# Kernel optimization log

Hardware: AMD Instinct MI355X
Metric: run time of the kernel (lower is better)

Reference implementation:

```python
import jax, jax.numpy as jnp
import numpy as np

L = 12        # depth
DIM = 768     # model dim
HEADS = 12
DHEAD = 64
INNER = HEADS * DHEAD   # 768
MLP = 3072
P = 16        # patch size
IMG = 384
C = 3
B = 16
NCLS = 1000
NPATCH = (IMG // P) ** 2   # 576
N = NPATCH + 1             # 577 (cls token)
PATCH_DIM = C * P * P      # 768
SCALE = DIM ** (-0.5)      # NOTE: original scales by dim, not dim_head


def setup_inputs() -> dict:
    key = jax.random.key(0)
    ks = jax.random.split(key, 21)
    rn = lambda k, shape, s=0.02: jax.random.normal(k, shape, dtype=jnp.float32) * s
    return {
        "img": jax.random.normal(ks[0], (B, C, IMG, IMG), dtype=jnp.float32),
        "patch_w": rn(ks[1], (PATCH_DIM, DIM)),
        "patch_b": rn(ks[2], (DIM,)),
        "pos_emb": rn(ks[3], (1, N, DIM), 1.0),
        "cls_tok": rn(ks[4], (1, 1, DIM), 1.0),
        "ln1_w": jnp.ones((L, DIM), jnp.float32),
        "ln1_b": jnp.zeros((L, DIM), jnp.float32),
        "qkv_w": rn(ks[5], (L, DIM, 3 * INNER)),
        "out_w": rn(ks[6], (L, INNER, DIM)),
        "out_b": rn(ks[7], (L, DIM)),
        "ln2_w": jnp.ones((L, DIM), jnp.float32),
        "ln2_b": jnp.zeros((L, DIM), jnp.float32),
        "ff1_w": rn(ks[8], (L, DIM, MLP)),
        "ff1_b": rn(ks[9], (L, MLP)),
        "ff2_w": rn(ks[10], (L, MLP, DIM)),
        "ff2_b": rn(ks[11], (L, DIM)),
        "head_ln_w": jnp.ones((DIM,), jnp.float32),
        "head_ln_b": jnp.zeros((DIM,), jnp.float32),
        "head_w": rn(ks[12], (DIM, NCLS)),
        "head_b": rn(ks[13], (NCLS,)),
    }


def layer_norm(x, w, b, eps=1e-5):
    mu = jnp.mean(x, axis=-1, keepdims=True)
    var = jnp.mean(jnp.square(x - mu), axis=-1, keepdims=True)
    return (x - mu) * jax.lax.rsqrt(var + eps) * w + b


def _vit_forward(img, patch_w, patch_b, pos_emb, cls_tok,
                 ln1_w, ln1_b, qkv_w, out_w, out_b,
                 ln2_w, ln2_b, ff1_w, ff1_b, ff2_w, ff2_b,
                 head_ln_w, head_ln_b, head_w, head_b):
    b = img.shape[0]
    g = IMG // P
    # rearrange 'b c (h p1) (w p2) -> b (h w) (p1 p2 c)'
    x = img.reshape(b, C, g, P, g, P).transpose(0, 2, 4, 3, 5, 1).reshape(b, NPATCH, PATCH_DIM)
    x = x @ patch_w + patch_b                           # [b, 576, dim]
    cls = jnp.broadcast_to(cls_tok, (b, 1, DIM))
    x = jnp.concatenate([cls, x], axis=1) + pos_emb[:, :N]   # [b, 577, dim]

    def block(x, p):
        l1w, l1b, qkvw, ow, ob, l2w, l2b, f1w, f1b, f2w, f2b = p
        # attention (pre-norm, residual inside Attention.forward)
        h = layer_norm(x, l1w, l1b)
        qkv = h @ qkvw                                  # [b, n, 3*inner]
        q, k, v = jnp.split(qkv, 3, axis=-1)
        to_heads = lambda t: t.reshape(b, N, HEADS, DHEAD).transpose(0, 2, 1, 3)
        q, k, v = to_heads(q), to_heads(k), to_heads(v)  # [b, h, n, d]
        dots = jnp.einsum('bhid,bhjd->bhij', q, k) * SCALE
        attn = jax.nn.softmax(dots, axis=-1)
        o = jnp.einsum('bhij,bhjd->bhid', attn, v)
        o = o.transpose(0, 2, 1, 3).reshape(b, N, INNER)
        x = x + (o @ ow + ob)
        # feedforward (pre-norm, residual)
        h2 = layer_norm(x, l2w, l2b)
        h2 = jax.nn.gelu(h2 @ f1w + f1b, approximate=False)
        x = x + (h2 @ f2w + f2b)
        return x, None

    x, _ = jax.lax.scan(block, x,
                        (ln1_w, ln1_b, qkv_w, out_w, out_b,
                         ln2_w, ln2_b, ff1_w, ff1_b, ff2_w, ff2_b))
    cls_out = x[:, 0]                                   # [b, dim]
    return layer_norm(cls_out, head_ln_w, head_ln_b) @ head_w + head_b


def reference(img, patch_w, patch_b, pos_emb, cls_tok,
              ln1_w, ln1_b, qkv_w, out_w, out_b,
              ln2_w, ln2_b, ff1_w, ff1_b, ff2_w, ff2_b,
              head_ln_w, head_ln_b, head_w, head_b):
    return _vit_forward(img, patch_w, patch_b, pos_emb, cls_tok,
                        ln1_w, ln1_b, qkv_w, out_w, out_b,
                        ln2_w, ln2_b, ff1_w, ff1_b, ff2_w, ff2_b,
                        head_ln_w, head_ln_b, head_w, head_b)
```

## Files before the change

### kernel.cpp

```cpp
#include <hip/hip_runtime.h>
#include <cstdint>


typedef __attribute__((ext_vector_type(8))) short bf16x8;
typedef __attribute__((ext_vector_type(4))) float f32x4;

#define NTOK 577

__device__ __forceinline__ ushort f2bf(float f) {
  union { float f; unsigned int u; } x; x.f = f;
  unsigned int r = x.u + 0x7fffu + ((x.u >> 16) & 1u);
  return (ushort)(r >> 16);
}

__device__ __forceinline__ void gload_lds16(const ushort* g, ushort* l) {
  __builtin_amdgcn_global_load_lds(
      (const __attribute__((address_space(1))) unsigned int*)g,
      (__attribute__((address_space(3))) unsigned int*)l, 16, 0, 0);
}

#define VMCNT4 asm volatile("s_waitcnt vmcnt(4)" ::: "memory")
#define VMCNT2 asm volatile("s_waitcnt vmcnt(2)" ::: "memory")
#define VMCNT0 asm volatile("s_waitcnt vmcnt(0)" ::: "memory")
#define LGKM0  asm volatile("s_waitcnt lgkmcnt(0)" ::: "memory")
#define SCHED0 __builtin_amdgcn_sched_barrier(0)
#define BARRIER __builtin_amdgcn_s_barrier()

__device__ __forceinline__ int gsw(int row) {
  return (row & 7) + 2 * ((row >> 4) & 3);
}

__device__ __forceinline__ void transpose_tile(const float* __restrict__ W,
                                               ushort* __restrict__ Wt,
                                               int K, int N, int kb, int nb,
                                               int tx, int ty, float t[32][33]) {
#pragma unroll
  for (int i = 0; i < 32; i += 8)
    t[ty + i][tx] = W[(size_t)(kb + ty + i) * N + (nb + tx)];
  __syncthreads();
#pragma unroll
  for (int i = 0; i < 32; i += 8)
    Wt[(size_t)(nb + ty + i) * K + (kb + tx)] = f2bf(t[tx][ty + i]);
}

__global__ __launch_bounds__(256) void convt_kernel(const float* __restrict__ W,
                                                    ushort* __restrict__ Wt,
                                                    int K, int N) {
  __shared__ float t[32][33];
  transpose_tile(W, Wt, K, N, blockIdx.x * 32, blockIdx.y * 32,
                 threadIdx.x & 31, threadIdx.x >> 5, t);
}

__global__ __launch_bounds__(256) void wconv_kernel(
    const float* __restrict__ qkv_w, const float* __restrict__ out_w,
    const float* __restrict__ ff1_w, const float* __restrict__ ff2_w,
    ushort* __restrict__ wq, ushort* __restrict__ wo,
    ushort* __restrict__ w1, ushort* __restrict__ w2) {
  __shared__ float t[32][33];
  const int tx = threadIdx.x & 31, ty = threadIdx.x >> 5;
  int bx = blockIdx.x;
  if (bx < 1728) {
    transpose_tile(qkv_w, wq, 768, 2304, (bx % 24) * 32, (bx / 24) * 32, tx, ty, t);
  } else if (bx < 2304) {
    bx -= 1728;
    transpose_tile(out_w, wo, 768, 768, (bx % 24) * 32, (bx / 24) * 32, tx, ty, t);
  } else if (bx < 4608) {
    bx -= 2304;
    transpose_tile(ff1_w, w1, 768, 3072, (bx % 24) * 32, (bx / 24) * 32, tx, ty, t);
  } else {
    bx -= 4608;
    transpose_tile(ff2_w, w2, 3072, 768, (bx % 96) * 32, (bx / 96) * 32, tx, ty, t);
  }
}

__global__ __launch_bounds__(256) void im2col_kernel(const float* __restrict__ img,
                                                     ushort* __restrict__ Ap) {
  const int idx = blockIdx.x * 256 + threadIdx.x;
  const int j = idx % 768;
  const int m = idx / 768;
  const int c = j % 3;
  const int q = j / 3;
  const int px = q & 15, py = q >> 4;
  const int b = m / 576, p = m % 576;
  const int gy = p / 24, gx = p % 24;
  const float v = img[((size_t)(b * 3 + c) * 384 + (gy * 16 + py)) * 384 + (gx * 16 + px)];
  Ap[idx] = f2bf(v);
}

__global__ void clspos_kernel(const float* __restrict__ cls_tok,
                              const float* __restrict__ pos,
                              float* __restrict__ x) {
  const int i = blockIdx.x * 256 + threadIdx.x;
  const int b = i / 768, d = i % 768;
  x[(size_t)b * NTOK * 768 + d] = cls_tok[d] + pos[d];
}

__global__ __launch_bounds__(256) void ln_kernel(const float* __restrict__ x,
                                                 const float* __restrict__ w,
                                                 const float* __restrict__ bb,
                                                 ushort* __restrict__ out) {
  const int wave = threadIdx.x >> 6, lane = threadIdx.x & 63;
  const int row = blockIdx.x * 4 + wave;
  const float4* xr = reinterpret_cast<const float4*>(x + (size_t)row * 768);
  const float4 v0 = xr[lane], v1 = xr[lane + 64], v2 = xr[lane + 128];
  float vals[12] = {v0.x, v0.y, v0.z, v0.w, v1.x, v1.y, v1.z, v1.w,
                    v2.x, v2.y, v2.z, v2.w};
  float s = 0.f;
#pragma unroll
  for (int i = 0; i < 12; ++i) s += vals[i];
#pragma unroll
  for (int o = 32; o; o >>= 1) s += __shfl_xor(s, o);
  const float mu = s * (1.0f / 768.0f);
  float q = 0.f;
#pragma unroll
  for (int i = 0; i < 12; ++i) { const float d = vals[i] - mu; q += d * d; }
#pragma unroll
  for (int o = 32; o; o >>= 1) q += __shfl_xor(q, o);
  const float rstd = rsqrtf(q * (1.0f / 768.0f) + 1e-5f);
  const float4* w4 = reinterpret_cast<const float4*>(w);
  const float4* b4 = reinterpret_cast<const float4*>(bb);
  ushort* orow = out + (size_t)row * 768;
#pragma unroll
  for (int ch = 0; ch < 3; ++ch) {
    const float4 wv = w4[lane + ch * 64];
    const float4 bv = b4[lane + ch * 64];
    ushort4 u;
    u.x = f2bf((vals[ch * 4 + 0] - mu) * rstd * wv.x + bv.x);
    u.y = f2bf((vals[ch * 4 + 1] - mu) * rstd * wv.y + bv.y);
    u.z = f2bf((vals[ch * 4 + 2] - mu) * rstd * wv.z + bv.z);
    u.w = f2bf((vals[ch * 4 + 3] - mu) * rstd * wv.w + bv.w);
    *reinterpret_cast<ushort4*>(orow + ch * 256 + lane * 4) = u;
  }
}

constexpr int EPI_BF16 = 0;
constexpr int EPI_GELU_BF16 = 1;
constexpr int EPI_RES_F32 = 2;
constexpr int EPI_PATCH = 3;

template <int EPI>
__global__ __launch_bounds__(512, 2) void gemm8_kernel(
    const ushort* __restrict__ A, const ushort* __restrict__ Bt,
    const float* __restrict__ bias, void* __restrict__ Cptr,
    int M, int N, int K, int nt) {
  __shared__ ushort lds[2][2][16384];

  const int nwg = gridDim.x;
  const int orig = blockIdx.x;
  const int q8 = nwg >> 3, r8 = nwg & 7, xcd = orig & 7, sidx = orig >> 3;
  const int wg = (xcd < r8 ? xcd * (q8 + 1) : r8 * (q8 + 1) + (xcd - r8) * q8) + sidx;
  const int tileM = (wg / nt) * 256;
  const int tileN = (wg % nt) * 256;

  const int tid = threadIdx.x;
  const int wave = tid >> 6, lane = tid & 63;
  const int wm = wave >> 2, wn = wave & 3;
  const int lr = lane & 15, lg = lane >> 4;

  f32x4 acc[8][4];
#pragma unroll
  for (int i = 0; i < 8; ++i)
#pragma unroll
    for (int j = 0; j < 4; ++j) acc[i][j] = (f32x4){0.f, 0.f, 0.f, 0.f};

  int rsA[2][2], rsB[2][2];
  const ushort* pA[2][2];
  const ushort* pB[2][2];
#pragma unroll
  for (int h = 0; h < 2; ++h)
#pragma unroll
    for (int g = 0; g < 2; ++g) {
      const int c = wave * 2 + g;
      {
        const int rowst = h * 64 + ((c >> 3) << 7) + ((c & 7) << 3);
        rsA[h][g] = rowst;
        const int row = rowst + (lane >> 3);
        const int lgr = ((lane & 7) - gsw(row)) & 7;
        pA[h][g] = A + (size_t)(tileM + row) * K + lgr * 8;
      }
      {
        const int rowst = h * 32 + ((c >> 2) << 6) + ((c & 3) << 3);
        rsB[h][g] = rowst;
        const int row = rowst + (lane >> 3);
        const int lgr = ((lane & 7) - gsw(row)) & 7;
        pB[h][g] = Bt + (size_t)(tileN + row) * K + lgr * 8;
      }
    }

#define STAGE_A(h, buf, k1)                                   \
  gload_lds16(pA[h][0] + (k1), &lds[buf][0][rsA[h][0] * 64]); \
  gload_lds16(pA[h][1] + (k1), &lds[buf][0][rsA[h][1] * 64]);
#define STAGE_B(h, buf, k1)                                   \
  gload_lds16(pB[h][0] + (k1), &lds[buf][1][rsB[h][0] * 64]); \
  gload_lds16(pB[h][1] + (k1), &lds[buf][1][rsB[h][1] * 64]);

  bf16x8 areg[8], breg[4];
#define LDA8(h, buf)                                                          \
  {                                                                           \
    const ushort* base = &lds[buf][0][0];                                     \
    _Pragma("unroll") for (int mf = 0; mf < 4; ++mf) {                        \
      const int row = wm * 128 + (h) * 64 + mf * 16 + lr;                     \
      _Pragma("unroll") for (int ks = 0; ks < 2; ++ks) {                      \
        const int pg = (ks * 4 + lg + (lr & 7) + 2 * mf) & 7;                 \
        areg[mf * 2 + ks] =                                                   \
            *reinterpret_cast<const bf16x8*>(&base[row * 64 + pg * 8]);       \
      }                                                                       \
    }                                                                         \
  }
#define LDB4(q, buf)                                                          \
  {                                                                           \
    const ushort* base = &lds[buf][1][0];                                     \
    _Pragma("unroll") for (int nf = 0; nf < 2; ++nf) {                        \
      const int row = wn * 64 + (q) * 32 + nf * 16 + lr;                      \
      _Pragma("unroll") for (int ks = 0; ks < 2; ++ks) {                      \
        const int pg = (ks * 4 + lg + (lr & 7) + 2 * (((q)*2 + nf) & 3)) & 7; \
        breg[nf * 2 + ks] =                                                   \
            *reinterpret_cast<const bf16x8*>(&base[row * 64 + pg * 8]);       \
      }                                                                       \
    }                                                                         \
  }
#define MFMA16(h, q)                                                        \
  __builtin_amdgcn_s_setprio(1);                                            \
  _Pragma("unroll") for (int mf = 0; mf < 4; ++mf)                          \
      _Pragma("unroll") for (int nf = 0; nf < 2; ++nf)                      \
          _Pragma("unroll") for (int ks = 0; ks < 2; ++ks)                  \
              acc[(h)*4 + mf][(q)*2 + nf] =                                 \
                  __builtin_amdgcn_mfma_f32_16x16x32_bf16(                  \
                      areg[mf * 2 + ks], breg[nf * 2 + ks],                 \
                      acc[(h)*4 + mf][(q)*2 + nf], 0, 0, 0);                \
  __builtin_amdgcn_s_setprio(0);

  STAGE_A(0, 0, 0);
  STAGE_B(0, 0, 0);
  STAGE_A(1, 0, 0);
  STAGE_B(1, 0, 0);

  const int NT = K >> 6;
  for (int t = 0; t < NT - 1; ++t) {
    const int cb = t & 1, nb = (t + 1) & 1;
    const int k1 = (t + 1) * 64;
    VMCNT4; SCHED0;
    BARRIER;
    LDA8(0, cb);
    LDB4(0, cb);
    STAGE_A(0, nb, k1);
    LGKM0; SCHED0;
    MFMA16(0, 0);
    VMCNT4; SCHED0;
    BARRIER;
    LDA8(1, cb);
    STAGE_B(0, nb, k1);
    LGKM0; SCHED0;
    MFMA16(1, 0);
    VMCNT4; SCHED0;
    BARRIER;
    LDB4(1, cb);
    STAGE_A(1, nb, k1);
    LGKM0; SCHED0;
    MFMA16(1, 1);
    BARRIER;
    LDA8(0, cb);
    STAGE_B(1, nb, k1);
    LGKM0; SCHED0;
    MFMA16(0, 1);
  }

  {
    const int cb = (NT - 1) & 1;
    VMCNT4; SCHED0;
    BARRIER;
    LDA8(0, cb);
    LDB4(0, cb);
    LGKM0; SCHED0;
    MFMA16(0, 0);
    VMCNT2; SCHED0;
    BARRIER;
    LDA8(1, cb);
    LGKM0; SCHED0;
    MFMA16(1, 0);
    VMCNT0; SCHED0;
    BARRIER;
    LDB4(1, cb);
    LGKM0; SCHED0;
    MFMA16(1, 1);
    BARRIER;
    LDA8(0, cb);
    LGKM0; SCHED0;
    MFMA16(0, 1);
  }

#pragma unroll
  for (int am = 0; am < 8; ++am) {
#pragma unroll
    for (int r = 0; r < 4; ++r) {
      const int row = tileM + wm * 128 + (am >> 2) * 64 + (am & 3) * 16 + lg * 4 + r;
      if (row >= M) continue;
#pragma unroll
      for (int an = 0; an < 4; ++an) {
        const int col = tileN + wn * 64 + (an >> 1) * 32 + (an & 1) * 16 + lr;
        float v = acc[am][an][r];
        if constexpr (EPI == EPI_BF16) {
          reinterpret_cast<ushort*>(Cptr)[(size_t)row * N + col] = f2bf(v);
        } else {
          v += bias[col];
          v = 0.5f * v * (1.0f + erff(v * 0.70710678118654752440f));
          reinterpret_cast<ushort*>(Cptr)[(size_t)row * N + col] = f2bf(v);
        }
      }
    }
  }
#undef STAGE_A
#undef STAGE_B
#undef LDA8
#undef LDB4
#undef MFMA16
}

template <int EPI>
__global__ __launch_bounds__(256) void gemmP_kernel(
    const ushort* __restrict__ A, const ushort* __restrict__ Bt,
    const float* __restrict__ bias, const float* __restrict__ extra,
    void* __restrict__ Cptr, int M, int N, int K, int mt) {
  __shared__ ushort ldsA[2][128 * 64];
  __shared__ ushort ldsB[2][128 * 64];

  const int nwg = gridDim.x;
  const int orig = blockIdx.x;
  const int q8 = nwg >> 3, r8 = nwg & 7, xcd = orig & 7, sidx = orig >> 3;
  const int wg = (xcd < r8 ? xcd * (q8 + 1) : r8 * (q8 + 1) + (xcd - r8) * q8) + sidx;
  const int tileM = (wg % mt) * 128;
  const int tileN = (wg / mt) * 128;

  const int tid = threadIdx.x;
  const int wave = tid >> 6, lane = tid & 63;
  const int wm = wave >> 1, wn = wave & 1;
  const int lr = lane & 15, lg = lane >> 4;

  f32x4 acc[4][4];
#pragma unroll
  for (int m = 0; m < 4; ++m)
#pragma unroll
    for (int n = 0; n < 4; ++n) acc[m][n] = (f32x4){0.f, 0.f, 0.f, 0.f};

  const ushort* pA[4];
  const ushort* pB[4];
  int dst[4];
#pragma unroll
  for (int i = 0; i < 4; ++i) {
    const int c = wave * 4 + i;
    const int rowst = c * 8;
    dst[i] = rowst * 64;
    const int row = rowst + (lane >> 3);
    const int lgr = ((lane & 7) - gsw(row)) & 7;
    pA[i] = A + (size_t)(tileM + row) * K + lgr * 8;
    pB[i] = Bt + (size_t)(tileN + row) * K + lgr * 8;
  }

#define PSTAGE(buf, kk)                              \
  _Pragma("unroll") for (int i = 0; i < 4; ++i)      \
      gload_lds16(pA[i] + (kk), &ldsA[buf][dst[i]]); \
  _Pragma("unroll") for (int i = 0; i < 4; ++i)      \
      gload_lds16(pB[i] + (kk), &ldsB[buf][dst[i]]);

  PSTAGE(0, 0);

  const int NT = K >> 6;
  int cb = 0;
  for (int t = 0; t < NT; ++t) {
    VMCNT0; SCHED0;
    BARRIER;
    if (t + 1 < NT) { PSTAGE(cb ^ 1, (t + 1) * 64); }
    bf16x8 a[8], b[8];
#pragma unroll
    for (int mf = 0; mf < 4; ++mf) {
      const int row = wm * 64 + mf * 16 + lr;
#pragma unroll
      for (int ks = 0; ks < 2; ++ks) {
        const int pg = (ks * 4 + lg + (lr & 7) + 2 * mf) & 7;
        a[mf * 2 + ks] = *reinterpret_cast<const bf16x8*>(&ldsA[cb][row * 64 + pg * 8]);
      }
    }
#pragma unroll
    for (int nf = 0; nf < 4; ++nf) {
      const int row = wn * 64 + nf * 16 + lr;
#pragma unroll
      for (int ks = 0; ks < 2; ++ks) {
        const int pg = (ks * 4 + lg + (lr & 7) + 2 * nf) & 7;
        b[nf * 2 + ks] = *reinterpret_cast<const bf16x8*>(&ldsB[cb][row * 64 + pg * 8]);
      }
    }
    LGKM0; SCHED0;
    __builtin_amdgcn_s_setprio(1);
#pragma unroll
    for (int mf = 0; mf < 4; ++mf)
#pragma unroll
      for (int nf = 0; nf < 4; ++nf)
#pragma unroll
        for (int ks = 0; ks < 2; ++ks)
          acc[mf][nf] = __builtin_amdgcn_mfma_f32_16x16x32_bf16(
              a[mf * 2 + ks], b[nf * 2 + ks], acc[mf][nf], 0, 0, 0);
    __builtin_amdgcn_s_setprio(0);
    cb ^= 1;
  }

#pragma unroll
  for (int mf = 0; mf < 4; ++mf) {
#pragma unroll
    for (int r = 0; r < 4; ++r) {
      const int row = tileM + wm * 64 + mf * 16 + lg * 4 + r;
      if (row >= M) continue;
#pragma unroll
      for (int nf = 0; nf < 4; ++nf) {
        const int col = tileN + wn * 64 + nf * 16 + lr;
        float v = acc[mf][nf][r];
        if constexpr (EPI == EPI_BF16) {
          reinterpret_cast<ushort*>(Cptr)[(size_t)row * N + col] = f2bf(v);
        } else if constexpr (EPI == EPI_GELU_BF16) {
          v += bias[col];
          v = 0.5f * v * (1.0f + erff(v * 0.70710678118654752440f));
          reinterpret_cast<ushort*>(Cptr)[(size_t)row * N + col] = f2bf(v);
        } else if constexpr (EPI == EPI_RES_F32) {
          v += bias[col] + extra[(size_t)row * N + col];
          reinterpret_cast<float*>(Cptr)[(size_t)row * N + col] = v;
        } else {
          const int bb = row / 576;
          const int p = row - bb * 576;
          v += bias[col] + extra[(size_t)(p + 1) * 768 + col];
          reinterpret_cast<float*>(Cptr)[(size_t)(row + bb + 1) * 768 + col] = v;
        }
      }
    }
  }
#undef PSTAGE
}

__global__ __launch_bounds__(256) void attn_kernel(const ushort* __restrict__ qkv,
                                                   ushort* __restrict__ o) {
  __shared__ ushort sK[64 * 64];
  __shared__ ushort sVt[64 * 64];
  __shared__ ushort sP[4][16 * 72];
  const int bh = blockIdx.x;
  const int b = bh / 12, hh = bh % 12;
  const int q0 = blockIdx.y * 64;
  const int tid = threadIdx.x;
  const int wave = tid >> 6, lane = tid & 63;
  const int lr = lane & 15;
  const int lg = lane >> 4;
  const ushort* base = qkv + (size_t)b * NTOK * 2304 + hh * 64;
  const float SC = 0.03608439182435161f;

  bf16x8 qf[2];
  {
    const int qrow = q0 + wave * 16 + lr;
    if (qrow < NTOK) {
      const ushort* qp = base + (size_t)qrow * 2304 + lg * 8;
      qf[0] = *reinterpret_cast<const bf16x8*>(qp);
      qf[1] = *reinterpret_cast<const bf16x8*>(qp + 32);
    } else {
      qf[0] = (bf16x8){0, 0, 0, 0, 0, 0, 0, 0};
      qf[1] = qf[0];
    }
  }

  float mst[4], lst[4];
  f32x4 oacc[4];
#pragma unroll
  for (int i = 0; i < 4; ++i) {
    mst[i] = -1e30f; lst[i] = 0.f;
    oacc[i] = (f32x4){0.f, 0.f, 0.f, 0.f};
  }

  const int skey = tid >> 2;
  const int sc4 = tid & 3;
  const int gswk = gsw(skey);

  for (int t0 = 0; t0 < NTOK; t0 += 64) {
    __syncthreads();
    {
      const int gk = t0 + skey;
      int4 k0v, k1v, v0v, v1v;
      if (gk < NTOK) {
        const int4* kp = reinterpret_cast<const int4*>(base + (size_t)gk * 2304 + 768 + sc4 * 16);
        k0v = kp[0]; k1v = kp[1];
        const int4* vp = reinterpret_cast<const int4*>(base + (size_t)gk * 2304 + 1536 + sc4 * 16);
        v0v = vp[0]; v1v = vp[1];
      } else {
        int4 z; z.x = z.y = z.z = z.w = 0;
        k0v = k1v = v0v = v1v = z;
      }
      *reinterpret_cast<int4*>(&sK[skey * 64 + (((2 * sc4 + 0) + gswk) & 7) * 8]) = k0v;
      *reinterpret_cast<int4*>(&sK[skey * 64 + (((2 * sc4 + 1) + gswk) & 7) * 8]) = k1v;
      const ushort* vs = reinterpret_cast<const ushort*>(&v0v);
      const ushort* vs2 = reinterpret_cast<const ushort*>(&v1v);
#pragma unroll
      for (int i = 0; i < 8; ++i) {
        const int d0 = sc4 * 16 + i;
        const int pg0 = ((skey >> 3) + gsw(d0)) & 7;
        sVt[d0 * 64 + pg0 * 8 + (skey & 7)] = vs[i];
        const int d1 = sc4 * 16 + 8 + i;
        const int pg1 = ((skey >> 3) + gsw(d1)) & 7;
        sVt[d1 * 64 + pg1 * 8 + (skey & 7)] = vs2[i];
      }
    }
    __syncthreads();

    f32x4 sacc[4];
#pragma unroll
    for (int n = 0; n < 4; ++n) sacc[n] = (f32x4){0.f, 0.f, 0.f, 0.f};
#pragma unroll
    for (int n = 0; n < 4; ++n) {
      const int row = n * 16 + lr;
      const int rot = (lr & 7) + 2 * n;
      const bf16x8 kf0 = *reinterpret_cast<const bf16x8*>(&sK[row * 64 + ((lg + rot) & 7) * 8]);
      const bf16x8 kf1 = *reinterpret_cast<const bf16x8*>(&sK[row * 64 + ((4 + lg + rot) & 7) * 8]);
      sacc[n] = __builtin_amdgcn_mfma_f32_16x16x32_bf16(qf[0], kf0, sacc[n], 0, 0, 0);
      sacc[n] = __builtin_amdgcn_mfma_f32_16x16x32_bf16(qf[1], kf1, sacc[n], 0, 0, 0);
    }

    float s[4][4], pm[4];
#pragma unroll
    for (int reg = 0; reg < 4; ++reg) pm[reg] = -1e30f;
#pragma unroll
    for (int n = 0; n < 4; ++n)
#pragma unroll
      for (int reg = 0; reg < 4; ++reg) {
        float v = sacc[n][reg] * SC;
        if (t0 + n * 16 + lr >= NTOK) v = -1e30f;
        s[n][reg] = v;
        pm[reg] = fmaxf(pm[reg], v);
      }
#pragma unroll
    for (int off = 1; off < 16; off <<= 1)
#pragma unroll
      for (int reg = 0; reg < 4; ++reg) pm[reg] = fmaxf(pm[reg], __shfl_xor(pm[reg], off));

    float al[4], rs[4];
#pragma unroll
    for (int reg = 0; reg < 4; ++reg) {
      const float mn = fmaxf(mst[reg], pm[reg]);
      al[reg] = __expf(mst[reg] - mn);
      mst[reg] = mn;
      rs[reg] = 0.f;
    }
#pragma unroll
    for (int n = 0; n < 4; ++n)
#pragma unroll
      for (int reg = 0; reg < 4; ++reg) {
        s[n][reg] = __expf(s[n][reg] - mst[reg]);
        rs[reg] += s[n][reg];
      }
#pragma unroll
    for (int off = 1; off < 16; off <<= 1)
#pragma unroll
      for (int reg = 0; reg < 4; ++reg) rs[reg] += __shfl_xor(rs[reg], off);
#pragma unroll
    for (int reg = 0; reg < 4; ++reg) {
      lst[reg] = lst[reg] * al[reg] + rs[reg];
#pragma unroll
      for (int n = 0; n < 4; ++n) oacc[n][reg] *= al[reg];
    }

#pragma unroll
    for (int n = 0; n < 4; ++n)
#pragma unroll
      for (int reg = 0; reg < 4; ++reg)
        sP[wave][(lg * 4 + reg) * 72 + n * 16 + lr] = f2bf(s[n][reg]);

    const bf16x8 pf0 = *reinterpret_cast<const bf16x8*>(&sP[wave][lr * 72 + lg * 8]);
    const bf16x8 pf1 = *reinterpret_cast<const bf16x8*>(&sP[wave][lr * 72 + 32 + lg * 8]);
#pragma unroll
    for (int n = 0; n < 4; ++n) {
      const int row = n * 16 + lr;
      const int rot = (lr & 7) + 2 * n;
      const bf16x8 vf0 = *reinterpret_cast<const bf16x8*>(&sVt[row * 64 + ((lg + rot) & 7) * 8]);
      const bf16x8 vf1 = *reinterpret_cast<const bf16x8*>(&sVt[row * 64 + ((4 + lg + rot) & 7) * 8]);
      oacc[n] = __builtin_amdgcn_mfma_f32_16x16x32_bf16(pf0, vf0, oacc[n], 0, 0, 0);
      oacc[n] = __builtin_amdgcn_mfma_f32_16x16x32_bf16(pf1, vf1, oacc[n], 0, 0, 0);
    }
  }

#pragma unroll
  for (int reg = 0; reg < 4; ++reg) {
    const int q = q0 + wave * 16 + lg * 4 + reg;
    if (q >= NTOK) continue;
    const float inv = 1.0f / lst[reg];
    ushort* op = o + (size_t)(b * NTOK + q) * 768 + hh * 64;
#pragma unroll
    for (int n = 0; n < 4; ++n) op[n * 16 + lr] = f2bf(oacc[n][reg] * inv);
  }
}

__global__ __launch_bounds__(256) void head_kernel(const float* __restrict__ x,
                                                   const float* __restrict__ lw,
                                                   const float* __restrict__ lb,
                                                   const float* __restrict__ hw,
                                                   const float* __restrict__ hb,
                                                   float* __restrict__ out) {
  __shared__ float srow[768];
  __shared__ float sred[8];
  const int b = blockIdx.x, tid = threadIdx.x;
  const float* xr = x + (size_t)b * NTOK * 768;
  for (int i = tid; i < 768; i += 256) srow[i] = xr[i];
  __syncthreads();
  float part = srow[tid] + srow[tid + 256] + srow[tid + 512];
#pragma unroll
  for (int off = 32; off; off >>= 1) part += __shfl_xor(part, off);
  if ((tid & 63) == 0) sred[tid >> 6] = part;
  __syncthreads();
  const float mu = (sred[0] + sred[1] + sred[2] + sred[3]) * (1.0f / 768.0f);
  const float d0 = srow[tid] - mu, d1 = srow[tid + 256] - mu, d2 = srow[tid + 512] - mu;
  float vp = d0 * d0 + d1 * d1 + d2 * d2;
#pragma unroll
  for (int off = 32; off; off >>= 1) vp += __shfl_xor(vp, off);
  if ((tid & 63) == 0) sred[4 + (tid >> 6)] = vp;
  __syncthreads();
  const float rstd = rsqrtf((sred[4] + sred[5] + sred[6] + sred[7]) * (1.0f / 768.0f) + 1e-5f);
  for (int i = tid; i < 768; i += 256) srow[i] = (srow[i] - mu) * rstd * lw[i] + lb[i];
  __syncthreads();
  const int c = blockIdx.y * 250 + tid;
  if (tid < 250 && c < 1000) {
    float a = 0.f;
#pragma unroll 4
    for (int k = 0; k < 768; ++k) a += srow[k] * hw[(size_t)k * 1000 + c];
    out[b * 1000 + c] = a + hb[c];
  }
}

extern "C" void kernel_launch(void* const* d_in, const int* in_sizes, int n_in,
                              void* d_out, int out_size, void* d_ws, size_t ws_size,
                              hipStream_t stream) {
  const float* img     = (const float*)d_in[0];
  const float* patch_w = (const float*)d_in[1];
  const float* patch_b = (const float*)d_in[2];
  const float* pos_emb = (const float*)d_in[3];
  const float* cls_tok = (const float*)d_in[4];
  const float* ln1_w   = (const float*)d_in[5];
  const float* ln1_b   = (const float*)d_in[6];
  const float* qkv_w   = (const float*)d_in[7];
  const float* out_w   = (const float*)d_in[8];
  const float* out_b   = (const float*)d_in[9];
  const float* ln2_w   = (const float*)d_in[10];
  const float* ln2_b   = (const float*)d_in[11];
  const float* ff1_w   = (const float*)d_in[12];
  const float* ff1_b   = (const float*)d_in[13];
  const float* ff2_w   = (const float*)d_in[14];
  const float* ff2_b   = (const float*)d_in[15];
  const float* hln_w   = (const float*)d_in[16];
  const float* hln_b   = (const float*)d_in[17];
  const float* head_w  = (const float*)d_in[18];
  const float* head_b  = (const float*)d_in[19];
  float* outp = (float*)d_out;

  char* wsp = (char*)d_ws;
  auto alloc = [&](size_t bytes) {
    char* p = wsp;
    wsp += (bytes + 255) & ~(size_t)255;
    return p;
  };
  float*  x    = (float*) alloc((size_t)9232 * 768 * 4);
  ushort* h    = (ushort*)alloc((size_t)9232 * 768 * 2);
  ushort* qkvb = (ushort*)alloc((size_t)9232 * 2304 * 2);
  ushort* mlp  = (ushort*)alloc((size_t)9232 * 3072 * 2);
  ushort* wq   = (ushort*)alloc((size_t)768 * 2304 * 2);
  ushort* wo   = (ushort*)alloc((size_t)768 * 768 * 2);
  ushort* w1   = (ushort*)alloc((size_t)768 * 3072 * 2);
  ushort* w2   = (ushort*)alloc((size_t)3072 * 768 * 2);
  ushort* apatch = mlp;
  ushort* wpatch = wq;

  convt_kernel<<<dim3(24, 24), 256, 0, stream>>>(patch_w, wpatch, 768, 768);
  im2col_kernel<<<27648, 256, 0, stream>>>(img, apatch);
  gemmP_kernel<EPI_PATCH><<<72 * 6, 256, 0, stream>>>(
      apatch, wpatch, patch_b, pos_emb, x, 9216, 768, 768, 72);
  clspos_kernel<<<48, 256, 0, stream>>>(cls_tok, pos_emb, x);

  for (int l = 0; l < 12; ++l) {
    wconv_kernel<<<6912, 256, 0, stream>>>(
        qkv_w + (size_t)l * 768 * 2304, out_w + (size_t)l * 768 * 768,
        ff1_w + (size_t)l * 768 * 3072, ff2_w + (size_t)l * 3072 * 768,
        wq, wo, w1, w2);
    ln_kernel<<<2308, 256, 0, stream>>>(x, ln1_w + l * 768, ln1_b + l * 768, h);
    gemm8_kernel<EPI_BF16><<<37 * 9, 512, 0, stream>>>(
        h, wq, nullptr, qkvb, 9232, 2304, 768, 9);
    attn_kernel<<<dim3(192, 10), 256, 0, stream>>>(qkvb, h);
    gemmP_kernel<EPI_RES_F32><<<73 * 6, 256, 0, stream>>>(
        h, wo, out_b + l * 768, x, x, 9232, 768, 768, 73);
    ln_kernel<<<2308, 256, 0, stream>>>(x, ln2_w + l * 768, ln2_b + l * 768, h);
    gemm8_kernel<EPI_GELU_BF16><<<37 * 12, 512, 0, stream>>>(
        h, w1, ff1_b + l * 3072, mlp, 9232, 3072, 768, 12);
    gemmP_kernel<EPI_RES_F32><<<73 * 6, 256, 0, stream>>>(
        mlp, w2, ff2_b + l * 768, x, x, 9232, 768, 3072, 73);
  }

  head_kernel<<<dim3(16, 4), 256, 0, stream>>>(x, hln_w, hln_b, head_w, head_b, outp);
}
```

Measured before the change: 4.171 ms.

## Restructure gemm8 main loop into two phases and split-K the head GEMV

The 8-wave GEMM main loop now loads all B fragments once per k-tile and issues two 32-MFMA phases instead of four 16-MFMA phases. This halves the barriers per tile and changes the global-to-LDS prefetch order and vmcnt waits to match. It adds breg register pressure, which may lower occupancy. Separately, the classifier head kernel splits K across four wave groups with an LDS reduction and launches more blocks, to get more parallelism on the small GEMV.

```diff
diff --git a/kernel.cpp b/kernel.cpp
--- a/kernel.cpp
+++ b/kernel.cpp
@@ -19,7 +19,7 @@
       (__attribute__((address_space(3))) unsigned int*)l, 16, 0, 0);
 }
 
-#define VMCNT4 asm volatile("s_waitcnt vmcnt(4)" ::: "memory")
+#define VMCNT6 asm volatile("s_waitcnt vmcnt(6)" ::: "memory")
 #define VMCNT2 asm volatile("s_waitcnt vmcnt(2)" ::: "memory")
 #define VMCNT0 asm volatile("s_waitcnt vmcnt(0)" ::: "memory")
 #define LGKM0  asm volatile("s_waitcnt lgkmcnt(0)" ::: "memory")
@@ -194,7 +194,7 @@
   gload_lds16(pB[h][0] + (k1), &lds[buf][1][rsB[h][0] * 64]); \
   gload_lds16(pB[h][1] + (k1), &lds[buf][1][rsB[h][1] * 64]);
 
-  bf16x8 areg[8], breg[4];
+  bf16x8 areg[8], breg[8];
 #define LDA8(h, buf)                                                          \
   {                                                                           \
     const ushort* base = &lds[buf][0][0];                                     \
@@ -207,86 +207,70 @@
       }                                                                       \
     }                                                                         \
   }
-#define LDB4(q, buf)                                                          \
+#define LDB8(buf)                                                             \
   {                                                                           \
     const ushort* base = &lds[buf][1][0];                                     \
-    _Pragma("unroll") for (int nf = 0; nf < 2; ++nf) {                        \
-      const int row = wn * 64 + (q) * 32 + nf * 16 + lr;                      \
+    _Pragma("unroll") for (int q = 0; q < 2; ++q)                             \
+        _Pragma("unroll") for (int nf = 0; nf < 2; ++nf) {                    \
+      const int row = wn * 64 + q * 32 + nf * 16 + lr;                        \
       _Pragma("unroll") for (int ks = 0; ks < 2; ++ks) {                      \
-        const int pg = (ks * 4 + lg + (lr & 7) + 2 * (((q)*2 + nf) & 3)) & 7; \
-        breg[nf * 2 + ks] =                                                   \
+        const int pg = (ks * 4 + lg + (lr & 7) + 2 * ((q * 2 + nf) & 3)) & 7; \
+        breg[q * 4 + nf * 2 + ks] =                                           \
             *reinterpret_cast<const bf16x8*>(&base[row * 64 + pg * 8]);       \
       }                                                                       \
     }                                                                         \
   }
-#define MFMA16(h, q)                                                        \
+#define MFMA32(h)                                                           \
   __builtin_amdgcn_s_setprio(1);                                            \
-  _Pragma("unroll") for (int mf = 0; mf < 4; ++mf)                          \
-      _Pragma("unroll") for (int nf = 0; nf < 2; ++nf)                      \
-          _Pragma("unroll") for (int ks = 0; ks < 2; ++ks)                  \
-              acc[(h)*4 + mf][(q)*2 + nf] =                                 \
-                  __builtin_amdgcn_mfma_f32_16x16x32_bf16(                  \
-                      areg[mf * 2 + ks], breg[nf * 2 + ks],                 \
-                      acc[(h)*4 + mf][(q)*2 + nf], 0, 0, 0);                \
+  _Pragma("unroll") for (int q = 0; q < 2; ++q)                             \
+      _Pragma("unroll") for (int mf = 0; mf < 4; ++mf)                      \
+          _Pragma("unroll") for (int nf = 0; nf < 2; ++nf)                  \
+              _Pragma("unroll") for (int ks = 0; ks < 2; ++ks)              \
+                  acc[(h)*4 + mf][q * 2 + nf] =                             \
+                      __builtin_amdgcn_mfma_f32_16x16x32_bf16(              \
+                          areg[mf * 2 + ks], breg[q * 4 + nf * 2 + ks],     \
+                          acc[(h)*4 + mf][q * 2 + nf], 0, 0, 0);            \
   __builtin_amdgcn_s_setprio(0);
 
   STAGE_A(0, 0, 0);
   STAGE_B(0, 0, 0);
+  STAGE_B(1, 0, 0);
   STAGE_A(1, 0, 0);
-  STAGE_B(1, 0, 0);
 
   const int NT = K >> 6;
   for (int t = 0; t < NT - 1; ++t) {
     const int cb = t & 1, nb = (t + 1) & 1;
     const int k1 = (t + 1) * 64;
-    VMCNT4; SCHED0;
+    VMCNT2; SCHED0;
     BARRIER;
     LDA8(0, cb);
-    LDB4(0, cb);
+    LDB8(cb);
     STAGE_A(0, nb, k1);
+    STAGE_B(0, nb, k1);
+    STAGE_B(1, nb, k1);
     LGKM0; SCHED0;
-    MFMA16(0, 0);
-    VMCNT4; SCHED0;
+    MFMA32(0);
+    VMCNT6; SCHED0;
     BARRIER;
     LDA8(1, cb);
-    STAGE_B(0, nb, k1);
-    LGKM0; SCHED0;
-    MFMA16(1, 0);
-    VMCNT4; SCHED0;
-    BARRIER;
-    LDB4(1, cb);
     STAGE_A(1, nb, k1);
     LGKM0; SCHED0;
-    MFMA16(1, 1);
+    MFMA32(1);
+  }
+
+  {
+    const int cb = (NT - 1) & 1;
+    VMCNT2; SCHED0;
     BARRIER;
     LDA8(0, cb);
-    STAGE_B(1, nb, k1);
+    LDB8(cb);
     LGKM0; SCHED0;
-    MFMA16(0, 1);
-  }
-
-  {
-    const int cb = (NT - 1) & 1;
-    VMCNT4; SCHED0;
-    BARRIER;
-    LDA8(0, cb);
-    LDB4(0, cb);
-    LGKM0; SCHED0;
-    MFMA16(0, 0);
-    VMCNT2; SCHED0;
+    MFMA32(0);
+    VMCNT0; SCHED0;
     BARRIER;
     LDA8(1, cb);
     LGKM0; SCHED0;
-    MFMA16(1, 0);
-    VMCNT0; SCHED0;
-    BARRIER;
-    LDB4(1, cb);
-    LGKM0; SCHED0;
-    MFMA16(1, 1);
-    BARRIER;
-    LDA8(0, cb);
-    LGKM0; SCHED0;
-    MFMA16(0, 1);
+    MFMA32(1);
   }
 
 #pragma unroll
@@ -312,8 +296,8 @@
 #undef STAGE_A
 #undef STAGE_B
 #undef LDA8
-#undef LDB4
-#undef MFMA16
+#undef LDB8
+#undef MFMA32
 }
 
 template <int EPI>
@@ -598,7 +582,8 @@
                                                    float* __restrict__ out) {
   __shared__ float srow[768];
   __shared__ float sred[8];
-  const int b = blockIdx.x, tid = threadIdx.x;
+  __shared__ float spart[4][64];
+  const int b = blockIdx.x, ct = blockIdx.y, tid = threadIdx.x;
   const float* xr = x + (size_t)b * NTOK * 768;
   for (int i = tid; i < 768; i += 256) srow[i] = xr[i];
   __syncthreads();
@@ -617,12 +602,21 @@
   const float rstd = rsqrtf((sred[4] + sred[5] + sred[6] + sred[7]) * (1.0f / 768.0f) + 1e-5f);
   for (int i = tid; i < 768; i += 256) srow[i] = (srow[i] - mu) * rstd * lw[i] + lb[i];
   __syncthreads();
-  const int c = blockIdx.y * 250 + tid;
-  if (tid < 250 && c < 1000) {
-    float a = 0.f;
-#pragma unroll 4
-    for (int k = 0; k < 768; ++k) a += srow[k] * hw[(size_t)k * 1000 + c];
-    out[b * 1000 + c] = a + hb[c];
+  const int cl = tid & 63, kq = tid >> 6;
+  const int c = ct * 64 + cl;
+  float a = 0.f;
+  if (c < 1000) {
+    const int k0 = kq * 192;
+#pragma unroll 8
+    for (int k = k0; k < k0 + 192; ++k) a += srow[k] * hw[(size_t)k * 1000 + c];
+  }
+  spart[kq][cl] = a;
+  __syncthreads();
+  if (tid < 64) {
+    const int c2 = ct * 64 + tid;
+    if (c2 < 1000)
+      out[b * 1000 + c2] =
+          spart[0][tid] + spart[1][tid] + spart[2][tid] + spart[3][tid] + hb[c2];
   }
 }
 
@@ -692,5 +686,5 @@
         mlp, w2, ff2_b + l * 768, x, x, 9232, 768, 3072, 73);
   }
 
-  head_kernel<<<dim3(16, 4), 256, 0, stream>>>(x, hln_w, hln_b, head_w, head_b, outp);
-}
+  head_kernel<<<dim3(16, 16), 256, 0, stream>>>(x, hln_w, hln_b, head_w, head_b, outp);
+}
```

Measured after the change: 4.051 ms (median of 2 runs). 1.03x faster.
